# Kernel tuning notes

Hardware: AMD Instinct MI355X
Metric: run time of the kernel (lower is better)

Reference implementation:

```python
import jax, jax.numpy as jnp
import numpy as np

N_NODES = 500_000
N_GRAPHS = 8192
HIDDEN = 256


def setup_inputs() -> dict:
    key = jax.random.key(0)
    k1, k2, k3, k4, k5, k6, k7 = jax.random.split(key, 7)
    h = jax.random.normal(k1, (N_NODES, HIDDEN), dtype=jnp.float32)
    node_mult = jax.random.uniform(k2, (N_NODES,), dtype=jnp.float32) * 3.0 + 0.5
    pressure = jax.random.uniform(k3, (N_GRAPHS,), dtype=jnp.float32) * 300.0
    attn_weight = jax.random.normal(k4, (HIDDEN,), dtype=jnp.float32) * (1.0 / np.sqrt(HIDDEN))
    attn_bias = jax.random.normal(k5, (1,), dtype=jnp.float32) * 0.01
    W_pressure = jax.random.normal(k6, (HIDDEN,), dtype=jnp.float32) * 0.02
    batch = jnp.sort(jax.random.randint(k7, (N_NODES,), 0, N_GRAPHS, dtype=jnp.int32))
    return {
        "h": h,
        "node_mult": node_mult,
        "pressure": pressure,
        "attn_weight": attn_weight,
        "attn_bias": attn_bias,
        "W_pressure": W_pressure,
        "batch": batch,
        "n_graphs": N_GRAPHS,
    }


def reference(h, node_mult, pressure, attn_weight, attn_bias, W_pressure, batch, n_graphs):
    # h: [N, H], node_mult: [N], batch: [N] int segment ids, pressure: [G]
    # Multiplicity-weighted mean pool
    total_mult = jax.ops.segment_sum(node_mult, batch, num_segments=n_graphs)  # [G]
    total_mult = jnp.maximum(total_mult, 1e-8)
    w_mean = node_mult / total_mult[batch]  # [N]
    mean_pool = jax.ops.segment_sum(h * w_mean[:, None], batch, num_segments=n_graphs)  # [G, H]

    # Segment max pool (empty segments -> -inf, matching torch full(-inf) init)
    max_pool = jax.ops.segment_max(h, batch, num_segments=n_graphs)  # [G, H]

    # Attention scores with log-multiplicity bias, then segment softmax
    raw_scores = h @ attn_weight + attn_bias[0] + jnp.log(jnp.maximum(node_mult, 1.0))  # [N]
    seg_max = jax.ops.segment_max(raw_scores, batch, num_segments=n_graphs)  # [G]
    exp_s = jnp.exp(raw_scores - seg_max[batch])  # [N]
    denom = jax.ops.segment_sum(exp_s, batch, num_segments=n_graphs)  # [G]
    attn_w = exp_s / denom[batch]  # [N]
    attn_pool = jax.ops.segment_sum(h * attn_w[:, None], batch, num_segments=n_graphs)  # [G, H]

    combined_mean = 0.5 * (mean_pool + attn_pool)  # [G, H]
    p_norm = (pressure / 300.0)[:, None]  # [G, 1]
    combined_mean = combined_mean + p_norm * W_pressure[None, :]
    return jnp.concatenate([combined_mean, max_pool], axis=-1)  # [G, 2H]
```

## Files before the change

kernel.cpp:

```cpp
#include <hip/hip_runtime.h>
#include <math.h>

#define HIDDEN 256
#define CHUNK 8

typedef float fx4 __attribute__((ext_vector_type(4)));

__global__ __launch_bounds__(256) void seg_starts_kernel(
    const int* __restrict__ batch, int* __restrict__ starts, int N, int G) {
  int i = blockIdx.x * blockDim.x + threadIdx.x;
  if (i >= N) return;
  int b = batch[i];
  int prev = (i == 0) ? -1 : batch[i - 1];
  for (int g = prev + 1; g <= b; ++g) starts[g] = i;
  if (i == N - 1) {
    for (int g = b + 1; g <= G; ++g) starts[g] = N;
  }
}

__global__ __launch_bounds__(256) void pool_kernel(
    const float* __restrict__ h, const float* __restrict__ node_mult,
    const float* __restrict__ pressure, const float* __restrict__ attn_weight,
    const float* __restrict__ attn_bias, const float* __restrict__ W_pressure,
    const int* __restrict__ starts, float* __restrict__ out, int G) {
  const int wave  = threadIdx.x >> 6;
  const int lane  = threadIdx.x & 63;
  const int gslot = wave >> 1;
  const int sub   = wave & 1;
  const int g = blockIdx.x * 2 + gslot;
  const bool active = (g < G);

  __shared__ float s_m[2], s_d[2], s_t[2];
  __shared__ fx4 s_attn[2][64], s_mean[2][64], s_max[2][64];

  int start = 0, end = 0;
  if (active) { start = starts[g]; end = starts[g + 1]; }
  const int total = end - start;
  const int nfull = total / CHUNK;
  const int rem   = total - nfull * CHUNK;

  const fx4 w4 = *reinterpret_cast<const fx4*>(attn_weight + 4 * lane);
  const float bias = attn_bias[0];

  fx4 attn  = (fx4)(0.f);
  fx4 meanv = (fx4)(0.f);
  fx4 maxv  = (fx4)(-INFINITY);
  float m = -INFINITY;
  float denom = 0.f;
  float tmult = 0.f;

  const int c_lo = (sub == 0) ? 0 : nfull / 2;
  const int c_hi = (sub == 0) ? nfull / 2 : nfull;

  for (int c = c_lo; c < c_hi; ++c) {
    const int i = start + c * CHUNK;
    fx4 hv[CHUNK];
    float mult[CHUNK];
#pragma unroll
    for (int j = 0; j < CHUNK; ++j) {
      hv[j] = __builtin_nontemporal_load(
          reinterpret_cast<const fx4*>(h + (size_t)(i + j) * HIDDEN + 4 * lane));
      mult[j] = node_mult[i + j];
    }

    float p[CHUNK];
#pragma unroll
    for (int j = 0; j < CHUNK; ++j)
      p[j] = hv[j].x * w4.x + hv[j].y * w4.y + hv[j].z * w4.z + hv[j].w * w4.w;

#pragma unroll
    for (int off = 32; off >= 1; off >>= 1) {
#pragma unroll
      for (int j = 0; j < CHUNK; ++j) p[j] += __shfl_xor(p[j], off, 64);
    }

    float s[CHUNK];
#pragma unroll
    for (int j = 0; j < CHUNK; ++j)
      s[j] = p[j] + bias + __logf(fmaxf(mult[j], 1.f));

    float cmax = s[0];
#pragma unroll
    for (int j = 1; j < CHUNK; ++j) cmax = fmaxf(cmax, s[j]);

    if (cmax > m) {
      const float scale = __expf(m - cmax);
      denom *= scale;
      attn *= scale;
      m = cmax;
    }

#pragma unroll
    for (int j = 0; j < CHUNK; ++j) {
      const float e = __expf(s[j] - m);
      denom += e;
      attn += hv[j] * e;
      meanv += hv[j] * mult[j];
      maxv.x = fmaxf(maxv.x, hv[j].x);  maxv.y = fmaxf(maxv.y, hv[j].y);
      maxv.z = fmaxf(maxv.z, hv[j].z);  maxv.w = fmaxf(maxv.w, hv[j].w);
      tmult += mult[j];
    }
  }

  if (sub == 0 && rem > 0) {
    const int base = start + nfull * CHUNK;
    fx4 hv[CHUNK];
    float mult[CHUNK];
#pragma unroll
    for (int j = 0; j < CHUNK; ++j) {
      const int idx = base + ((j < rem) ? j : rem - 1);
      hv[j] = __builtin_nontemporal_load(
          reinterpret_cast<const fx4*>(h + (size_t)idx * HIDDEN + 4 * lane));
      mult[j] = (j < rem) ? node_mult[base + j] : 0.f;
    }

    float p[CHUNK];
#pragma unroll
    for (int j = 0; j < CHUNK; ++j)
      p[j] = hv[j].x * w4.x + hv[j].y * w4.y + hv[j].z * w4.z + hv[j].w * w4.w;

#pragma unroll
    for (int off = 32; off >= 1; off >>= 1) {
#pragma unroll
      for (int j = 0; j < CHUNK; ++j) p[j] += __shfl_xor(p[j], off, 64);
    }

    float s[CHUNK];
#pragma unroll
    for (int j = 0; j < CHUNK; ++j)
      s[j] = (j < rem) ? (p[j] + bias + __logf(fmaxf(mult[j], 1.f))) : -INFINITY;

    float cmax = s[0];
#pragma unroll
    for (int j = 1; j < CHUNK; ++j) cmax = fmaxf(cmax, s[j]);

    if (cmax > m) {
      const float scale = __expf(m - cmax);
      denom *= scale;
      attn *= scale;
      m = cmax;
    }

#pragma unroll
    for (int j = 0; j < CHUNK; ++j) {
      const float e = __expf(s[j] - m);
      denom += e;
      attn += hv[j] * e;
      meanv += hv[j] * mult[j];
      const bool v = (j < rem);
      maxv.x = fmaxf(maxv.x, v ? hv[j].x : -INFINITY);
      maxv.y = fmaxf(maxv.y, v ? hv[j].y : -INFINITY);
      maxv.z = fmaxf(maxv.z, v ? hv[j].z : -INFINITY);
      maxv.w = fmaxf(maxv.w, v ? hv[j].w : -INFINITY);
      tmult += mult[j];
    }
  }

  if (sub == 1) {
    if (lane == 0) { s_m[gslot] = m; s_d[gslot] = denom; s_t[gslot] = tmult; }
    s_attn[gslot][lane] = attn;
    s_mean[gslot][lane] = meanv;
    s_max[gslot][lane]  = maxv;
  }
  __syncthreads();

  if (active && sub == 0) {
    const float m1 = s_m[gslot], d1 = s_d[gslot], t1 = s_t[gslot];
    const fx4 attn1 = s_attn[gslot][lane];
    const fx4 mean1 = s_mean[gslot][lane];
    const fx4 max1  = s_max[gslot][lane];

    const float M = fmaxf(m, m1);
    const float sc0 = (m  == -INFINITY) ? 0.f : __expf(m  - M);
    const float sc1 = (m1 == -INFINITY) ? 0.f : __expf(m1 - M);
    const float D = denom * sc0 + d1 * sc1;
    const fx4 A = attn * sc0 + attn1 * sc1;
    const fx4 Me = meanv + mean1;
    fx4 Mx;
    Mx.x = fmaxf(maxv.x, max1.x);  Mx.y = fmaxf(maxv.y, max1.y);
    Mx.z = fmaxf(maxv.z, max1.z);  Mx.w = fmaxf(maxv.w, max1.w);
    const float T = tmult + t1;

    const float inv_tm  = 1.f / fmaxf(T, 1e-8f);
    const float inv_den = (D > 0.f) ? 1.f / D : 0.f;
    const float p_norm  = pressure[g] * (1.f / 300.f);
    const fx4 wp4 = *reinterpret_cast<const fx4*>(W_pressure + 4 * lane);

    fx4 res = 0.5f * (Me * inv_tm + A * inv_den) + p_norm * wp4;

    float* outg = out + (size_t)g * (2 * HIDDEN);
    *reinterpret_cast<fx4*>(outg + 4 * lane) = res;
    *reinterpret_cast<fx4*>(outg + HIDDEN + 4 * lane) = Mx;
  }
}

extern "C" void kernel_launch(void* const* d_in, const int* in_sizes, int n_in,
                              void* d_out, int out_size, void* d_ws, size_t ws_size,
                              hipStream_t stream) {
  const float* h           = (const float*)d_in[0];
  const float* node_mult   = (const float*)d_in[1];
  const float* pressure    = (const float*)d_in[2];
  const float* attn_weight = (const float*)d_in[3];
  const float* attn_bias   = (const float*)d_in[4];
  const float* W_pressure  = (const float*)d_in[5];
  const int*   batch       = (const int*)d_in[6];

  const int N = in_sizes[1];
  const int G = in_sizes[2];

  int* starts = (int*)d_ws;
  float* out = (float*)d_out;

  seg_starts_kernel<<<(N + 255) / 256, 256, 0, stream>>>(batch, starts, N, G);
  pool_kernel<<<(G + 1) / 2, 256, 0, stream>>>(h, node_mult, pressure,
                                               attn_weight, attn_bias,
                                               W_pressure, starts, out, G);
}
```

Before: 100.4 us.

## Split each graph segment across four waves with shared-memory merge

Each block now handles one graph with four waves, each taking a quarter of the chunk range, where before two waves shared a graph and each block held two graphs. The partial tail chunk goes to whichever wave's range contains it, instead of always wave 0, which balances the load better. The intent is more memory-level parallelism per segment and shorter per-wave serial chains, since segments average about 61 nodes. The cost is a grid of G blocks and a three-way online-softmax merge in shared memory, with more waves sitting idle on small segments.

```diff
diff --git a/kernel.cpp b/kernel.cpp
--- a/kernel.cpp
+++ b/kernel.cpp
@@ -23,21 +23,19 @@
     const float* __restrict__ pressure, const float* __restrict__ attn_weight,
     const float* __restrict__ attn_bias, const float* __restrict__ W_pressure,
     const int* __restrict__ starts, float* __restrict__ out, int G) {
-  const int wave  = threadIdx.x >> 6;
-  const int lane  = threadIdx.x & 63;
-  const int gslot = wave >> 1;
-  const int sub   = wave & 1;
-  const int g = blockIdx.x * 2 + gslot;
-  const bool active = (g < G);
-
-  __shared__ float s_m[2], s_d[2], s_t[2];
-  __shared__ fx4 s_attn[2][64], s_mean[2][64], s_max[2][64];
-
-  int start = 0, end = 0;
-  if (active) { start = starts[g]; end = starts[g + 1]; }
+  const int q    = threadIdx.x >> 6;
+  const int lane = threadIdx.x & 63;
+  const int g = blockIdx.x;
+
+  __shared__ float s_m[3], s_d[3], s_t[3];
+  __shared__ fx4 s_attn[3][64], s_mean[3][64], s_max[3][64];
+
+  const int start = starts[g];
+  const int end   = starts[g + 1];
   const int total = end - start;
   const int nfull = total / CHUNK;
   const int rem   = total - nfull * CHUNK;
+  const int nt    = nfull + (rem > 0);
 
   const fx4 w4 = *reinterpret_cast<const fx4*>(attn_weight + 4 * lane);
   const float bias = attn_bias[0];
@@ -49,10 +47,11 @@
   float denom = 0.f;
   float tmult = 0.f;
 
-  const int c_lo = (sub == 0) ? 0 : nfull / 2;
-  const int c_hi = (sub == 0) ? nfull / 2 : nfull;
-
-  for (int c = c_lo; c < c_hi; ++c) {
+  const int c_lo = (q * nt) / 4;
+  const int c_hi = ((q + 1) * nt) / 4;
+  const int f_hi = (c_hi < nfull) ? c_hi : nfull;
+
+  for (int c = c_lo; c < f_hi; ++c) {
     const int i = start + c * CHUNK;
     fx4 hv[CHUNK];
     float mult[CHUNK];
@@ -102,7 +101,7 @@
     }
   }
 
-  if (sub == 0 && rem > 0) {
+  if (rem > 0 && c_lo <= nfull && nfull < c_hi) {
     const int base = start + nfull * CHUNK;
     fx4 hv[CHUNK];
     float mult[CHUNK];
@@ -156,30 +155,32 @@
     }
   }
 
-  if (sub == 1) {
-    if (lane == 0) { s_m[gslot] = m; s_d[gslot] = denom; s_t[gslot] = tmult; }
-    s_attn[gslot][lane] = attn;
-    s_mean[gslot][lane] = meanv;
-    s_max[gslot][lane]  = maxv;
+  if (q > 0) {
+    if (lane == 0) { s_m[q - 1] = m; s_d[q - 1] = denom; s_t[q - 1] = tmult; }
+    s_attn[q - 1][lane] = attn;
+    s_mean[q - 1][lane] = meanv;
+    s_max[q - 1][lane]  = maxv;
   }
   __syncthreads();
 
-  if (active && sub == 0) {
-    const float m1 = s_m[gslot], d1 = s_d[gslot], t1 = s_t[gslot];
-    const fx4 attn1 = s_attn[gslot][lane];
-    const fx4 mean1 = s_mean[gslot][lane];
-    const fx4 max1  = s_max[gslot][lane];
-
-    const float M = fmaxf(m, m1);
-    const float sc0 = (m  == -INFINITY) ? 0.f : __expf(m  - M);
-    const float sc1 = (m1 == -INFINITY) ? 0.f : __expf(m1 - M);
-    const float D = denom * sc0 + d1 * sc1;
-    const fx4 A = attn * sc0 + attn1 * sc1;
-    const fx4 Me = meanv + mean1;
-    fx4 Mx;
-    Mx.x = fmaxf(maxv.x, max1.x);  Mx.y = fmaxf(maxv.y, max1.y);
-    Mx.z = fmaxf(maxv.z, max1.z);  Mx.w = fmaxf(maxv.w, max1.w);
-    const float T = tmult + t1;
+  if (q == 0) {
+    float M = m, D = denom, T = tmult;
+    fx4 A = attn, Me = meanv, Mx = maxv;
+#pragma unroll
+    for (int k = 0; k < 3; ++k) {
+      const float mk = s_m[k];
+      const float Mn = fmaxf(M, mk);
+      const float sc0 = (M  == -INFINITY) ? 0.f : __expf(M  - Mn);
+      const float sck = (mk == -INFINITY) ? 0.f : __expf(mk - Mn);
+      D = D * sc0 + s_d[k] * sck;
+      A = A * sc0 + s_attn[k][lane] * sck;
+      M = Mn;
+      Me += s_mean[k][lane];
+      const fx4 mxk = s_max[k][lane];
+      Mx.x = fmaxf(Mx.x, mxk.x);  Mx.y = fmaxf(Mx.y, mxk.y);
+      Mx.z = fmaxf(Mx.z, mxk.z);  Mx.w = fmaxf(Mx.w, mxk.w);
+      T += s_t[k];
+    }
 
     const float inv_tm  = 1.f / fmaxf(T, 1e-8f);
     const float inv_den = (D > 0.f) ? 1.f / D : 0.f;
@@ -212,7 +213,7 @@
   float* out = (float*)d_out;
 
   seg_starts_kernel<<<(N + 255) / 256, 256, 0, stream>>>(batch, starts, N, G);
-  pool_kernel<<<(G + 1) / 2, 256, 0, stream>>>(h, node_mult, pressure,
-                                               attn_weight, attn_bias,
-                                               W_pressure, starts, out, G);
+  pool_kernel<<<G, 256, 0, stream>>>(h, node_mult, pressure,
+                                     attn_weight, attn_bias,
+                                     W_pressure, starts, out, G);
 }
```

Result: faster. 98.26 us (-2.1%).
